# Kernel optimization log

Hardware: AMD Instinct MI355X
Metric: run time of the kernel (lower is better)

The kernel has to match this reference:

```python
import jax, jax.numpy as jnp
import numpy as np

NL, DM, DI, DS, DC, DR, NC = 4, 128, 256, 16, 4, 8, 10
ALPHA = 0.3  # observer_alpha

def layernorm(x, w, b, eps=1e-5):
    m = x.mean(-1, keepdims=True)
    v = ((x - m) ** 2).mean(-1, keepdims=True)
    return (x - m) / jnp.sqrt(v + eps) * w + b

def silu(x):
    return x * jax.nn.sigmoid(x)

def causal_dwconv(x, w, b):
    # x: (B, L, DI); w: (DI, 1, DC); b: (DI,)
    xt = x.transpose(0, 2, 1)  # (B, DI, L)
    y = jax.lax.conv_general_dilated(
        xt, w, window_strides=(1,), padding=[(DC - 1, 0)],
        dimension_numbers=('NCH', 'OIH', 'NCH'), feature_group_count=DI)
    return (y + b[None, :, None]).transpose(0, 2, 1)  # (B, L, DI)

def ssm_scan(delta, Bc, Cc, u, A):
    # delta, u: (B, L, DI); Bc, Cc: (B, L, DS); A: (DI, DS)
    B = delta.shape[0]
    def step(h, inp):
        d_t, b_t, c_t, u_t = inp  # (B,DI),(B,DS),(B,DS),(B,DI)
        dA = jnp.exp(d_t[..., None] * A)              # (B, DI, DS)
        h = dA * h + (d_t * u_t)[..., None] * b_t[:, None, :]
        y = jnp.einsum('bds,bs->bd', h, c_t)
        return h, y
    h0 = jnp.zeros((B, DI, DS), delta.dtype)
    xs = (delta.transpose(1, 0, 2), Bc.transpose(1, 0, 2),
          Cc.transpose(1, 0, 2), u.transpose(1, 0, 2))
    _, ys = jax.lax.scan(step, h0, xs)
    return ys.transpose(1, 0, 2)  # (B, L, DI)

def _forward(x, W_in, b_in, ln_w, ln_b, in_proj_w, conv_w, conv_b, x_proj_w,
             dt_proj_w, dt_proj_b, A_log, Dp, out_proj_w, out_proj_b,
             norm_w, norm_b, cls_w, cls_b):
    B = x.shape[0]
    u = x.transpose(0, 2, 3, 1).reshape(B, -1, 3)   # (B, L, 3)
    h = u @ W_in + b_in                              # (B, L, DM)
    for i in range(NL):
        res = h
        z = layernorm(h, ln_w[i], ln_b[i])
        xz = z @ in_proj_w[i]                        # (B, L, 2*DI)
        xin, gate = jnp.split(xz, 2, axis=-1)
        xc = silu(causal_dwconv(xin, conv_w[i], conv_b[i]))  # (B, L, DI)
        proj = xc @ x_proj_w[i]                      # (B, L, DR + 2*DS)
        dt, Bc, Cc = jnp.split(proj, [DR, DR + DS], axis=-1)
        delta = jax.nn.softplus(dt @ dt_proj_w[i] + dt_proj_b[i])  # (B, L, DI)
        A = -jnp.exp(A_log[i])                       # (DI, DS)
        y = ssm_scan(delta, Bc, Cc, xc, A) + xc * Dp[i]
        # Luenberger-style observer correction: blend predicted SSM output
        y = (1.0 - ALPHA) * y + ALPHA * xc
        y = y * silu(gate)
        h = res + y @ out_proj_w[i] + out_proj_b[i]
    pooled = h.mean(axis=1)                          # (B, DM)
    pooled = layernorm(pooled, norm_w, norm_b)
    return pooled @ cls_w + cls_b                    # (B, NC)

def setup_inputs():
    key = jax.random.key(0)
    ks = jax.random.split(key, 8)
    def nrm(k, shape, std=0.02):
        return jax.random.normal(k, shape, jnp.float32) * std
    return {
        'x': jax.random.normal(ks[0], (32, 3, 32, 32), jnp.float32),
        'W_in': nrm(ks[1], (3, DM)), 'b_in': jnp.zeros((DM,), jnp.float32),
        'ln_w': jnp.ones((NL, DM), jnp.float32), 'ln_b': jnp.zeros((NL, DM), jnp.float32),
        'in_proj_w': nrm(ks[2], (NL, DM, 2 * DI)),
        'conv_w': nrm(ks[3], (NL, DI, 1, DC), 0.2), 'conv_b': jnp.zeros((NL, DI), jnp.float32),
        'x_proj_w': nrm(ks[4], (NL, DI, DR + 2 * DS)),
        'dt_proj_w': nrm(ks[5], (NL, DR, DI), 0.1),
        'dt_proj_b': jnp.full((NL, DI), -4.6, jnp.float32),
        'A_log': jnp.log(jnp.broadcast_to(jnp.arange(1, DS + 1, dtype=jnp.float32), (NL, DI, DS))),
        'Dp': jnp.ones((NL, DI), jnp.float32),
        'out_proj_w': nrm(ks[6], (NL, DI, DM)), 'out_proj_b': jnp.zeros((NL, DM), jnp.float32),
        'norm_w': jnp.ones((DM,), jnp.float32), 'norm_b': jnp.zeros((DM,), jnp.float32),
        'cls_w': nrm(ks[7], (DM, NC)), 'cls_b': jnp.zeros((NC,), jnp.float32),
    }

def reference(x, W_in, b_in, ln_w, ln_b, in_proj_w, conv_w, conv_b, x_proj_w,
              dt_proj_w, dt_proj_b, A_log, Dp, out_proj_w, out_proj_b,
              norm_w, norm_b, cls_w, cls_b):
    return _forward(x, W_in, b_in, ln_w, ln_b, in_proj_w, conv_w, conv_b,
                    x_proj_w, dt_proj_w, dt_proj_b, A_log, Dp, out_proj_w,
                    out_proj_b, norm_w, norm_b, cls_w, cls_b)
```

## Files before the change

### kernel.cpp

```cpp
#include <hip/hip_runtime.h>
#include <math.h>

#define B_  32
#define L_  1024
#define T_  (B_ * L_)
#define DM_ 128
#define DI_ 256
#define DS_ 16
#define DC_ 4
#define DR_ 8
#define NC_ 10
#define CHUNK_ 32
#define NCH_  (L_ / CHUNK_)
#define PSTR_ 288

typedef __bf16 bf16x8 __attribute__((ext_vector_type(8)));
typedef __bf16 bf16x4 __attribute__((ext_vector_type(4)));
typedef __bf16 bf16x2 __attribute__((ext_vector_type(2)));
typedef float f32x4 __attribute__((ext_vector_type(4)));
typedef unsigned short u16x8 __attribute__((ext_vector_type(8)));

__device__ __forceinline__ float sigmoidf_(float x) { return 1.0f / (1.0f + __expf(-x)); }
__device__ __forceinline__ float siluf_(float x)    { return x * sigmoidf_(x); }
__device__ __forceinline__ float softplusf_(float x) {
    return (x > 15.0f) ? x : __logf(1.0f + __expf(x));
}
__device__ __forceinline__ float fexp2_(float x) { return __builtin_amdgcn_exp2f(x); }

__device__ __forceinline__ void gload_lds16(const __bf16* g, __bf16* l) {
    __builtin_amdgcn_global_load_lds(
        (const __attribute__((address_space(1))) void*)g,
        (__attribute__((address_space(3))) void*)l, 16, 0, 0);
}

template<int R>
__device__ __forceinline__ void stage_async(const __bf16* __restrict__ src,
        __bf16* lds, int k0, int stride, int wid, int lane) {
    constexpr int NI = R / 32;
#pragma unroll
    for (int j = 0; j < NI; ++j) {
        int s0 = (wid * NI + j) * 64;
        int s = s0 + lane;
        int row = s >> 3, sw = s & 7;
        int slot = sw ^ (row & 7);
        gload_lds16(src + (size_t)row * stride + k0 + slot * 8, lds + (size_t)s0 * 8);
    }
}

__global__ __launch_bounds__(128) void k_embed(const float* __restrict__ x,
        const float* __restrict__ Win, const float* __restrict__ bin,
        float* __restrict__ h) {
    int t = blockIdx.x;
    int b = t >> 10, l = t & 1023;
    int m = threadIdx.x;
    const float* xb = x + (size_t)b * 3 * 1024 + l;
    float acc = bin[m];
    acc = fmaf(xb[0],    Win[m],        acc);
    acc = fmaf(xb[1024], Win[128 + m],  acc);
    acc = fmaf(xb[2048], Win[256 + m],  acc);
    h[(size_t)t * 128 + m] = acc;
}

__global__ __launch_bounds__(256) void k_prep(const float* __restrict__ ipw,
        const float* __restrict__ opw, const float* __restrict__ xpw,
        const float* __restrict__ dtw, __bf16* __restrict__ wt1,
        __bf16* __restrict__ wt2, __bf16* __restrict__ wcat) {
    int blk = blockIdx.x;
    int tid = threadIdx.x;
    int i = blk * 256 + tid;
    if (i < 262144) {
        int lay = i >> 16, rem = i & 65535, n = rem >> 7, k = rem & 127;
        wt1[i] = (__bf16)ipw[lay * 65536 + k * 512 + n];
    }
    if (i < 131072) {
        int lay = i >> 15, rem = i & 32767, n = rem >> 8, k = rem & 255;
        wt2[i] = (__bf16)opw[lay * 32768 + k * 128 + n];
    }
    {
        int lay = blk / 384, n = blk % 384;
        int k = tid;
        float v;
        if (n < 256) {
            float acc = 0.0f;
#pragma unroll
            for (int r = 0; r < 8; ++r)
                acc = fmaf(xpw[lay * 10240 + k * 40 + r], dtw[lay * 2048 + r * 256 + n], acc);
            v = acc;
        } else if (n < 288) {
            v = xpw[lay * 10240 + k * 40 + (n - 248)];
        } else {
            v = 0.0f;
        }
        wcat[(size_t)blk * 256 + k] = (__bf16)v;
    }
}

__global__ __launch_bounds__(256) void k_ln(const float* __restrict__ h,
        const float* __restrict__ w, const float* __restrict__ b,
        __bf16* __restrict__ z) {
    int wid = threadIdx.x >> 6, lane = threadIdx.x & 63;
    int t = blockIdx.x * 4 + wid;
    const float* hr = h + (size_t)t * 128;
    float2 v = *(const float2*)(hr + lane * 2);
    float s = v.x + v.y, sq = v.x * v.x + v.y * v.y;
#pragma unroll
    for (int off = 1; off < 64; off <<= 1) {
        s += __shfl_xor(s, off);
        sq += __shfl_xor(sq, off);
    }
    float mean = s * (1.0f / 128.0f);
    float var = sq * (1.0f / 128.0f) - mean * mean;
    float rstd = rsqrtf(var + 1e-5f);
    float2 wv = *(const float2*)(w + lane * 2);
    float2 bv = *(const float2*)(b + lane * 2);
    bf16x2 o;
    o.x = (__bf16)((v.x - mean) * rstd * wv.x + bv.x);
    o.y = (__bf16)((v.y - mean) * rstd * wv.y + bv.y);
    *(bf16x2*)(z + (size_t)t * 128 + lane * 2) = o;
}

template<int BM, int K, int N, int MODE, bool GATE, bool WLN>
__global__ __launch_bounds__(256) void k_gemm_mfma(
        const __bf16* __restrict__ A, const __bf16* __restrict__ G,
        const __bf16* __restrict__ Wt, const float* __restrict__ bias,
        float* __restrict__ Cf, __bf16* __restrict__ Cb,
        const float* __restrict__ lnw, const float* __restrict__ lnb,
        __bf16* __restrict__ Zb) {
    static_assert(!GATE || BM == 32, "GATE staging assumes BM=32");
    static_assert(!WLN || (MODE == 2 && BM == 32 && N == 128), "WLN geometry");
    __shared__ __bf16 As[BM * 64];
    __shared__ __bf16 Bs[128 * 64];
    __shared__ float red_s[WLN ? 4 : 1][WLN ? 32 : 1];
    __shared__ float red_q[WLN ? 4 : 1][WLN ? 32 : 1];
    int tid = threadIdx.x;
    int bm = blockIdx.x, bn = blockIdx.y;
    int lane = tid & 63, wid = tid >> 6;
    int lr = lane & 15, lg = lane >> 4;
    constexpr int MF = BM / 16;

    f32x4 acc[MF][2] = {};
    const __bf16* Asrc = A + (size_t)(bm * BM) * K;
    const __bf16* Bsrc = Wt + (size_t)(bn * 128) * K;

    for (int k0 = 0; k0 < K; k0 += 64) {
        if (GATE) {
            int row = tid >> 3, slot = tid & 7;
            int m = bm * BM + row;
            bf16x8 yv = *(const bf16x8*)(A + (size_t)m * K + k0 + slot * 8);
            bf16x8 gv = *(const bf16x8*)(G + (size_t)m * 512 + 256 + k0 + slot * 8);
            bf16x8 v;
#pragma unroll
            for (int j = 0; j < 8; ++j)
                v[j] = (__bf16)((float)yv[j] * siluf_((float)gv[j]));
            *(bf16x8*)(As + row * 64 + ((slot ^ (row & 7)) * 8)) = v;
        } else {
            stage_async<BM>(Asrc, As, k0, K, wid, lane);
        }
        stage_async<128>(Bsrc, Bs, k0, K, wid, lane);
        __syncthreads();
#pragma unroll
        for (int ks = 0; ks < 2; ++ks) {
            int slotbase = ks * 4 + lg;
            bf16x8 af[MF], bfr[2];
#pragma unroll
            for (int m = 0; m < MF; ++m) {
                int row = m * 16 + lr;
                af[m] = *(const bf16x8*)(As + row * 64 + ((slotbase ^ (row & 7)) * 8));
            }
#pragma unroll
            for (int n = 0; n < 2; ++n) {
                int rn = wid * 32 + n * 16 + lr;
                bfr[n] = *(const bf16x8*)(Bs + rn * 64 + ((slotbase ^ (rn & 7)) * 8));
            }
#pragma unroll
            for (int m = 0; m < MF; ++m)
#pragma unroll
                for (int n = 0; n < 2; ++n)
                    acc[m][n] = __builtin_amdgcn_mfma_f32_16x16x32_bf16(
                        af[m], bfr[n], acc[m][n], 0, 0, 0);
        }
        __syncthreads();
    }
    float vv[MF][2][4];
#pragma unroll
    for (int m = 0; m < MF; ++m) {
#pragma unroll
        for (int n = 0; n < 2; ++n) {
            int col = bn * 128 + wid * 32 + n * 16 + lr;
            float bv = (MODE == 2) ? bias[col] : 0.0f;
            float dtbv = (MODE == 1 && col < 256) ? bias[col] : 0.0f;
#pragma unroll
            for (int rg = 0; rg < 4; ++rg) {
                int row = bm * BM + m * 16 + lg * 4 + rg;
                float v = acc[m][n][rg];
                if (MODE == 0) {
                    Cb[(size_t)row * N + col] = (__bf16)v;
                } else if (MODE == 1) {
                    if (col < 256)
                        Cb[(size_t)row * PSTR_ + col] = (__bf16)softplusf_(v + dtbv);
                    else if (col < 288)
                        Cb[(size_t)row * PSTR_ + col] = (__bf16)v;
                } else {
                    float* cp = Cf + (size_t)row * N + col;
                    v += *cp + bv;
                    *cp = v;
                    vv[m][n][rg] = v;
                }
            }
        }
    }
    if (WLN) {
        float ps[MF][4], pq[MF][4];
#pragma unroll
        for (int m = 0; m < MF; ++m)
#pragma unroll
            for (int rg = 0; rg < 4; ++rg) {
                float a = vv[m][0][rg], bv2 = vv[m][1][rg];
                ps[m][rg] = a + bv2;
                pq[m][rg] = a * a + bv2 * bv2;
            }
#pragma unroll
        for (int off = 1; off < 16; off <<= 1) {
#pragma unroll
            for (int m = 0; m < MF; ++m)
#pragma unroll
                for (int rg = 0; rg < 4; ++rg) {
                    ps[m][rg] += __shfl_xor(ps[m][rg], off);
                    pq[m][rg] += __shfl_xor(pq[m][rg], off);
                }
        }
        if (lr == 0) {
#pragma unroll
            for (int m = 0; m < MF; ++m)
#pragma unroll
                for (int rg = 0; rg < 4; ++rg) {
                    int rl = m * 16 + lg * 4 + rg;
                    red_s[wid][rl] = ps[m][rg];
                    red_q[wid][rl] = pq[m][rg];
                }
        }
        __syncthreads();
#pragma unroll
        for (int m = 0; m < MF; ++m)
#pragma unroll
            for (int rg = 0; rg < 4; ++rg) {
                int rl = m * 16 + lg * 4 + rg;
                float s = red_s[0][rl] + red_s[1][rl] + red_s[2][rl] + red_s[3][rl];
                float q = red_q[0][rl] + red_q[1][rl] + red_q[2][rl] + red_q[3][rl];
                float mean = s * (1.0f / 128.0f);
                float var = q * (1.0f / 128.0f) - mean * mean;
                float rstd = rsqrtf(var + 1e-5f);
#pragma unroll
                for (int n = 0; n < 2; ++n) {
                    int col = wid * 32 + n * 16 + lr;
                    float z = (vv[m][n][rg] - mean) * rstd * lnw[col] + lnb[col];
                    Zb[(size_t)(bm * BM + rl) * 128 + col] = (__bf16)z;
                }
            }
    }
}

__global__ __launch_bounds__(256) void k_conv(const __bf16* __restrict__ xzb,
        const float* __restrict__ cw, const float* __restrict__ cb,
        __bf16* __restrict__ xcb) {
    int t = blockIdx.x * 4 + (threadIdx.x >> 6);
    int d0 = (threadIdx.x & 63) * 4;
    int l = t & 1023;
    const __bf16* xp = xzb + (size_t)t * 512 + d0;
    float4 wv[4];
#pragma unroll
    for (int j = 0; j < 4; ++j) wv[j] = *(const float4*)(cw + (d0 + j) * 4);
    float acc[4] = {cb[d0], cb[d0 + 1], cb[d0 + 2], cb[d0 + 3]};
#pragma unroll
    for (int k = 0; k < 4; ++k) {
        int back = 3 - k;
        if (l >= back) {
            bf16x4 v = *(const bf16x4*)(xp - back * 512);
#pragma unroll
            for (int j = 0; j < 4; ++j)
                acc[j] = fmaf((float)v[j], ((const float*)&wv[j])[k], acc[j]);
        }
    }
    bf16x4 o;
#pragma unroll
    for (int j = 0; j < 4; ++j) o[j] = (__bf16)siluf_(acc[j]);
    *(bf16x4*)(xcb + (size_t)t * 256 + d0) = o;
}

template<bool FINAL>
__global__ __launch_bounds__(128) void k_scan_chunk(
        const __bf16* __restrict__ projall, const __bf16* __restrict__ xcb,
        const float* __restrict__ Alog, const float* __restrict__ Dp,
        float* __restrict__ P, float* __restrict__ S,
        __bf16* __restrict__ yb) {
    __shared__ unsigned du_lds[CHUNK_ * 128];
    __shared__ float bc[CHUNK_ * 32];
    int b = blockIdx.z, c = blockIdx.y, dg = blockIdx.x;
    int tid = threadIdx.x;
    int d = dg * 128 + tid;

    const __bf16* projC = projall + ((size_t)b * 1024 + c * CHUNK_) * PSTR_;
    const __bf16* xcC   = xcb + ((size_t)b * 1024 + c * CHUNK_) * 256 + dg * 128;

#pragma unroll
    for (int r = 0; r < (CHUNK_ * 16) / 128; ++r) {
        int item = r * 128 + tid;
        int t = item >> 4, o8 = (item & 15) * 8;
        u16x8 dv = *(const u16x8*)(projC + (size_t)t * PSTR_ + dg * 128 + o8);
        u16x8 xv = *(const u16x8*)(xcC + (size_t)t * 256 + o8);
        uint4 w0, w1;
        w0.x = dv[0] | ((unsigned)xv[0] << 16); w0.y = dv[1] | ((unsigned)xv[1] << 16);
        w0.z = dv[2] | ((unsigned)xv[2] << 16); w0.w = dv[3] | ((unsigned)xv[3] << 16);
        w1.x = dv[4] | ((unsigned)xv[4] << 16); w1.y = dv[5] | ((unsigned)xv[5] << 16);
        w1.z = dv[6] | ((unsigned)xv[6] << 16); w1.w = dv[7] | ((unsigned)xv[7] << 16);
        *(uint4*)(du_lds + t * 128 + o8)     = w0;
        *(uint4*)(du_lds + t * 128 + o8 + 4) = w1;
    }
#pragma unroll
    for (int r = 0; r < (CHUNK_ * 4) / 128; ++r) {
        int item = r * 128 + tid;
        int t = item >> 2, g8 = (item & 3) * 8;
        bf16x8 v = *(const bf16x8*)(projC + (size_t)t * PSTR_ + 256 + g8);
        float4 f0 = {(float)v[0], (float)v[1], (float)v[2], (float)v[3]};
        float4 f1 = {(float)v[4], (float)v[5], (float)v[6], (float)v[7]};
        *(float4*)(bc + t * 32 + g8)     = f0;
        *(float4*)(bc + t * 32 + g8 + 4) = f1;
    }

    float aa[16], hs[16];
#pragma unroll
    for (int jj = 0; jj < 4; ++jj) {
        float4 av = *(const float4*)(Alog + (size_t)d * 16 + jj * 4);
        aa[jj * 4 + 0] = -__expf(av.x) * 1.44269504088896f;
        aa[jj * 4 + 1] = -__expf(av.y) * 1.44269504088896f;
        aa[jj * 4 + 2] = -__expf(av.z) * 1.44269504088896f;
        aa[jj * 4 + 3] = -__expf(av.w) * 1.44269504088896f;
    }
    float Dpd = Dp[d];
    size_t psIdx = ((size_t)(b * NCH_ + c)) * 4096 + (size_t)d * 16;
    if (FINAL) {
#pragma unroll
        for (int jj = 0; jj < 4; ++jj) {
            float4 h0 = *(const float4*)(P + psIdx + jj * 4);
            hs[jj * 4 + 0] = h0.x; hs[jj * 4 + 1] = h0.y;
            hs[jj * 4 + 2] = h0.z; hs[jj * 4 + 3] = h0.w;
        }
    } else {
#pragma unroll
        for (int j = 0; j < 16; ++j) hs[j] = 0.0f;
    }
    float cumd = 0.0f;
    __bf16* yC = yb + ((size_t)b * 1024 + c * CHUNK_) * 256 + dg * 128 + tid;

    __syncthreads();
#pragma unroll 2
    for (int tt = 0; tt < CHUNK_; ++tt) {
        unsigned duv = du_lds[tt * 128 + tid];
        float delta_t = __uint_as_float(duv << 16);
        float u = __uint_as_float(duv & 0xffff0000u);
        float du = delta_t * u;
        const float* bcr = bc + tt * 32;
        if (!FINAL) cumd += delta_t;
        float ys = 0.0f;
#pragma unroll
        for (int jj = 0; jj < 4; ++jj) {
            float4 Bv = *(const float4*)(bcr + jj * 4);
            float4 Cv;
            if (FINAL) Cv = *(const float4*)(bcr + 16 + jj * 4);
#pragma unroll
            for (int j = 0; j < 4; ++j) {
                int s = jj * 4 + j;
                float dA = fexp2_(delta_t * aa[s]);
                hs[s] = fmaf(dA, hs[s], du * ((const float*)&Bv)[j]);
                if (FINAL) ys = fmaf(hs[s], ((const float*)&Cv)[j], ys);
            }
        }
        if (FINAL) {
            float yv = fmaf(u, Dpd, ys);
            yv = fmaf(0.7f, yv, 0.3f * u);
            yC[(size_t)tt * 256] = (__bf16)yv;
        }
    }
    if (!FINAL) {
#pragma unroll
        for (int jj = 0; jj < 4; ++jj) {
            float4 pv, sv;
            pv.x = fexp2_(aa[jj * 4 + 0] * cumd);
            pv.y = fexp2_(aa[jj * 4 + 1] * cumd);
            pv.z = fexp2_(aa[jj * 4 + 2] * cumd);
            pv.w = fexp2_(aa[jj * 4 + 3] * cumd);
            sv.x = hs[jj * 4 + 0]; sv.y = hs[jj * 4 + 1];
            sv.z = hs[jj * 4 + 2]; sv.w = hs[jj * 4 + 3];
            *(float4*)(P + psIdx + jj * 4) = pv;
            *(float4*)(S + psIdx + jj * 4) = sv;
        }
    }
}

__global__ __launch_bounds__(256) void k_scan_combine(float* __restrict__ P,
        const float* __restrict__ S) {
    int idx = blockIdx.x * 256 + threadIdx.x;
    int b = idx >> 12, rem = idx & 4095;
    float h = 0.0f;
#pragma unroll
    for (int c = 0; c < NCH_; ++c) {
        size_t base = ((size_t)(b * NCH_ + c)) * 4096 + rem;
        float p = P[base];
        float s = S[base];
        P[base] = h;
        h = fmaf(p, h, s);
    }
}

__global__ __launch_bounds__(128) void k_pool(const float* __restrict__ h,
        float* __restrict__ partial) {
    int b = blockIdx.x, lc = blockIdx.y;
    int m = threadIdx.x;
    const float* hb = h + (size_t)b * 131072 + (size_t)lc * 128 * 128 + m;
    float acc = 0.0f;
#pragma unroll 8
    for (int l = 0; l < 128; ++l) acc += hb[(size_t)l * 128];
    partial[((size_t)b * 8 + lc) * 128 + m] = acc;
}

__global__ __launch_bounds__(128) void k_head(const float* __restrict__ partial,
        const float* __restrict__ nw, const float* __restrict__ nb,
        const float* __restrict__ cw, const float* __restrict__ cb,
        float* __restrict__ out) {
    __shared__ float zs[128];
    __shared__ float red[128];
    int b = blockIdx.x, m = threadIdx.x;
    float v = 0.0f;
#pragma unroll
    for (int lc = 0; lc < 8; ++lc) v += partial[((size_t)b * 8 + lc) * 128 + m];
    v *= (1.0f / 1024.0f);
    red[m] = v;
    __syncthreads();
    for (int off = 64; off; off >>= 1) {
        if (m < off) red[m] += red[m + off];
        __syncthreads();
    }
    float mean = red[0] * (1.0f / 128.0f);
    __syncthreads();
    float dv = v - mean;
    red[m] = dv * dv;
    __syncthreads();
    for (int off = 64; off; off >>= 1) {
        if (m < off) red[m] += red[m + off];
        __syncthreads();
    }
    float rstd = rsqrtf(red[0] * (1.0f / 128.0f) + 1e-5f);
    zs[m] = dv * rstd * nw[m] + nb[m];
    __syncthreads();
    if (m < NC_) {
        float acc = cb[m];
#pragma unroll 8
        for (int k = 0; k < 128; ++k) acc = fmaf(zs[k], cw[k * 10 + m], acc);
        out[b * 10 + m] = acc;
    }
}

extern "C" void kernel_launch(void* const* d_in, const int* in_sizes, int n_in,
                              void* d_out, int out_size, void* d_ws, size_t ws_size,
                              hipStream_t stream) {
    const float* x    = (const float*)d_in[0];
    const float* Win  = (const float*)d_in[1];
    const float* bin  = (const float*)d_in[2];
    const float* lnw  = (const float*)d_in[3];
    const float* lnb  = (const float*)d_in[4];
    const float* ipw  = (const float*)d_in[5];
    const float* cw   = (const float*)d_in[6];
    const float* cb   = (const float*)d_in[7];
    const float* xpw  = (const float*)d_in[8];
    const float* dtw  = (const float*)d_in[9];
    const float* dtb  = (const float*)d_in[10];
    const float* Alog = (const float*)d_in[11];
    const float* Dp   = (const float*)d_in[12];
    const float* opw  = (const float*)d_in[13];
    const float* opb  = (const float*)d_in[14];
    const float* nw   = (const float*)d_in[15];
    const float* nb   = (const float*)d_in[16];
    const float* clw  = (const float*)d_in[17];
    const float* clb  = (const float*)d_in[18];

    float* ws = (float*)d_ws;
    float*  h       = ws;
    float*  P       = ws + 4194304;
    __bf16* zb      = (__bf16*)(ws + 4194304);
    __bf16* xzb     = (__bf16*)(ws + 8388608);
    __bf16* xcb     = (__bf16*)(ws + 16777216);
    __bf16* projall = (__bf16*)(ws + 20971520);
    __bf16* yb      = (__bf16*)(ws + 25690112);
    float*  partial = ws + 29884416;
    __bf16* wt1     = (__bf16*)(ws + 29917184);
    __bf16* wt2     = (__bf16*)(ws + 30048256);
    __bf16* wcat    = (__bf16*)(ws + 30113792);
    float*  Sb      = ws + 30310400;

    k_prep<<<1536, 256, 0, stream>>>(ipw, opw, xpw, dtw, wt1, wt2, wcat);
    k_embed<<<T_, 128, 0, stream>>>(x, Win, bin, h);
    k_ln<<<T_ / 4, 256, 0, stream>>>(h, lnw, lnb, zb);
    for (int lay = 0; lay < 4; ++lay) {
        k_gemm_mfma<64, 128, 512, 0, false, false><<<dim3(T_ / 64, 4), 256, 0, stream>>>(
            zb, nullptr, wt1 + (size_t)lay * 65536, nullptr, nullptr, xzb,
            nullptr, nullptr, nullptr);
        k_conv<<<T_ / 4, 256, 0, stream>>>(xzb, cw + lay * 1024, cb + lay * 256, xcb);
        k_gemm_mfma<64, 256, 384, 1, false, false><<<dim3(T_ / 64, 3), 256, 0, stream>>>(
            xcb, nullptr, wcat + (size_t)lay * 98304, dtb + lay * 256, nullptr, projall,
            nullptr, nullptr, nullptr);
        k_scan_chunk<false><<<dim3(2, NCH_, B_), 128, 0, stream>>>(projall, xcb,
            Alog + lay * 4096, Dp + lay * 256, P, Sb, yb);
        k_scan_combine<<<B_ * 4096 / 256, 256, 0, stream>>>(P, Sb);
        k_scan_chunk<true><<<dim3(2, NCH_, B_), 128, 0, stream>>>(projall, xcb,
            Alog + lay * 4096, Dp + lay * 256, P, Sb, yb);
        if (lay < 3) {
            k_gemm_mfma<32, 256, 128, 2, true, true><<<dim3(T_ / 32, 1), 256, 0, stream>>>(
                yb, xzb, wt2 + (size_t)lay * 32768, opb + lay * 128, h, nullptr,
                lnw + (lay + 1) * 128, lnb + (lay + 1) * 128, zb);
        } else {
            k_gemm_mfma<32, 256, 128, 2, true, false><<<dim3(T_ / 32, 1), 256, 0, stream>>>(
                yb, xzb, wt2 + (size_t)lay * 32768, opb + lay * 128, h, nullptr,
                nullptr, nullptr, nullptr);
        }
    }
    k_pool<<<dim3(32, 8), 128, 0, stream>>>(h, partial);
    k_head<<<32, 128, 0, stream>>>(partial, nw, nb, clw, clb, (float*)d_out);
}
```

Measured before the change: 617.2 us.

## Double-buffer LDS tiles in non-gated MFMA GEMM to overlap loads with compute

After: 617.4 us. Within noise of the previous version (+0.0%).

```diff
diff --git a/kernel.cpp b/kernel.cpp
--- a/kernel.cpp
+++ b/kernel.cpp
@@ -128,8 +128,9 @@
         __bf16* __restrict__ Zb) {
     static_assert(!GATE || BM == 32, "GATE staging assumes BM=32");
     static_assert(!WLN || (MODE == 2 && BM == 32 && N == 128), "WLN geometry");
-    __shared__ __bf16 As[BM * 64];
-    __shared__ __bf16 Bs[128 * 64];
+    constexpr int NBUF = GATE ? 1 : 2;
+    __shared__ __bf16 As[NBUF][BM * 64];
+    __shared__ __bf16 Bs[NBUF][128 * 64];
     __shared__ float red_s[WLN ? 4 : 1][WLN ? 32 : 1];
     __shared__ float red_q[WLN ? 4 : 1][WLN ? 32 : 1];
     int tid = threadIdx.x;
@@ -142,44 +143,83 @@
     const __bf16* Asrc = A + (size_t)(bm * BM) * K;
     const __bf16* Bsrc = Wt + (size_t)(bn * 128) * K;
 
-    for (int k0 = 0; k0 < K; k0 += 64) {
-        if (GATE) {
-            int row = tid >> 3, slot = tid & 7;
-            int m = bm * BM + row;
-            bf16x8 yv = *(const bf16x8*)(A + (size_t)m * K + k0 + slot * 8);
-            bf16x8 gv = *(const bf16x8*)(G + (size_t)m * 512 + 256 + k0 + slot * 8);
-            bf16x8 v;
-#pragma unroll
-            for (int j = 0; j < 8; ++j)
-                v[j] = (__bf16)((float)yv[j] * siluf_((float)gv[j]));
-            *(bf16x8*)(As + row * 64 + ((slot ^ (row & 7)) * 8)) = v;
-        } else {
-            stage_async<BM>(Asrc, As, k0, K, wid, lane);
-        }
-        stage_async<128>(Bsrc, Bs, k0, K, wid, lane);
-        __syncthreads();
-#pragma unroll
-        for (int ks = 0; ks < 2; ++ks) {
-            int slotbase = ks * 4 + lg;
-            bf16x8 af[MF], bfr[2];
-#pragma unroll
-            for (int m = 0; m < MF; ++m) {
-                int row = m * 16 + lr;
-                af[m] = *(const bf16x8*)(As + row * 64 + ((slotbase ^ (row & 7)) * 8));
-            }
-#pragma unroll
-            for (int n = 0; n < 2; ++n) {
-                int rn = wid * 32 + n * 16 + lr;
-                bfr[n] = *(const bf16x8*)(Bs + rn * 64 + ((slotbase ^ (rn & 7)) * 8));
-            }
-#pragma unroll
-            for (int m = 0; m < MF; ++m)
-#pragma unroll
-                for (int n = 0; n < 2; ++n)
-                    acc[m][n] = __builtin_amdgcn_mfma_f32_16x16x32_bf16(
-                        af[m], bfr[n], acc[m][n], 0, 0, 0);
-        }
-        __syncthreads();
+    if (!GATE) {
+        stage_async<BM>(Asrc, As[0], 0, K, wid, lane);
+        stage_async<128>(Bsrc, Bs[0], 0, K, wid, lane);
+        asm volatile("s_waitcnt vmcnt(0)" ::: "memory");
+        __builtin_amdgcn_s_barrier();
+        __builtin_amdgcn_sched_barrier(0);
+        int cur = 0;
+        for (int k0 = 0; k0 < K; k0 += 64) {
+            if (k0 + 64 < K) {
+                stage_async<BM>(Asrc, As[cur ^ 1], k0 + 64, K, wid, lane);
+                stage_async<128>(Bsrc, Bs[cur ^ 1], k0 + 64, K, wid, lane);
+            }
+            __builtin_amdgcn_sched_barrier(0);
+#pragma unroll
+            for (int ks = 0; ks < 2; ++ks) {
+                int slotbase = ks * 4 + lg;
+                bf16x8 af[MF], bfr[2];
+#pragma unroll
+                for (int m = 0; m < MF; ++m) {
+                    int row = m * 16 + lr;
+                    af[m] = *(const bf16x8*)(As[cur] + row * 64 + ((slotbase ^ (row & 7)) * 8));
+                }
+#pragma unroll
+                for (int n = 0; n < 2; ++n) {
+                    int rn = wid * 32 + n * 16 + lr;
+                    bfr[n] = *(const bf16x8*)(Bs[cur] + rn * 64 + ((slotbase ^ (rn & 7)) * 8));
+                }
+#pragma unroll
+                for (int m = 0; m < MF; ++m)
+#pragma unroll
+                    for (int n = 0; n < 2; ++n)
+                        acc[m][n] = __builtin_amdgcn_mfma_f32_16x16x32_bf16(
+                            af[m], bfr[n], acc[m][n], 0, 0, 0);
+            }
+            asm volatile("s_waitcnt vmcnt(0) lgkmcnt(0)" ::: "memory");
+            __builtin_amdgcn_s_barrier();
+            __builtin_amdgcn_sched_barrier(0);
+            cur ^= 1;
+        }
+    } else {
+        for (int k0 = 0; k0 < K; k0 += 64) {
+            {
+                int row = tid >> 3, slot = tid & 7;
+                int m = bm * BM + row;
+                bf16x8 yv = *(const bf16x8*)(A + (size_t)m * K + k0 + slot * 8);
+                bf16x8 gv = *(const bf16x8*)(G + (size_t)m * 512 + 256 + k0 + slot * 8);
+                bf16x8 v;
+#pragma unroll
+                for (int j = 0; j < 8; ++j)
+                    v[j] = (__bf16)((float)yv[j] * siluf_((float)gv[j]));
+                *(bf16x8*)(As[0] + row * 64 + ((slot ^ (row & 7)) * 8)) = v;
+            }
+            stage_async<128>(Bsrc, Bs[0], k0, K, wid, lane);
+            __syncthreads();
+#pragma unroll
+            for (int ks = 0; ks < 2; ++ks) {
+                int slotbase = ks * 4 + lg;
+                bf16x8 af[MF], bfr[2];
+#pragma unroll
+                for (int m = 0; m < MF; ++m) {
+                    int row = m * 16 + lr;
+                    af[m] = *(const bf16x8*)(As[0] + row * 64 + ((slotbase ^ (row & 7)) * 8));
+                }
+#pragma unroll
+                for (int n = 0; n < 2; ++n) {
+                    int rn = wid * 32 + n * 16 + lr;
+                    bfr[n] = *(const bf16x8*)(Bs[0] + rn * 64 + ((slotbase ^ (rn & 7)) * 8));
+                }
+#pragma unroll
+                for (int m = 0; m < MF; ++m)
+#pragma unroll
+                    for (int n = 0; n < 2; ++n)
+                        acc[m][n] = __builtin_amdgcn_mfma_f32_16x16x32_bf16(
+                            af[m], bfr[n], acc[m][n], 0, 0, 0);
+            }
+            __syncthreads();
+        }
     }
     float vv[MF][2][4];
 #pragma unroll
```

## Compute delta projection inside scan; shrink x_proj GEMM and pre-silu gate

Applied to the files above, without the earlier changes.

Result: no change. 621.2 us (+0.6%).

```diff
diff --git a/kernel.cpp b/kernel.cpp
--- a/kernel.cpp
+++ b/kernel.cpp
@@ -12,13 +12,12 @@
 #define NC_ 10
 #define CHUNK_ 32
 #define NCH_  (L_ / CHUNK_)
-#define PSTR_ 288
+#define PSTR_ 64
 
 typedef __bf16 bf16x8 __attribute__((ext_vector_type(8)));
 typedef __bf16 bf16x4 __attribute__((ext_vector_type(4)));
 typedef __bf16 bf16x2 __attribute__((ext_vector_type(2)));
 typedef float f32x4 __attribute__((ext_vector_type(4)));
-typedef unsigned short u16x8 __attribute__((ext_vector_type(8)));
 
 __device__ __forceinline__ float sigmoidf_(float x) { return 1.0f / (1.0f + __expf(-x)); }
 __device__ __forceinline__ float siluf_(float x)    { return x * sigmoidf_(x); }
@@ -63,12 +62,12 @@
 
 __global__ __launch_bounds__(256) void k_prep(const float* __restrict__ ipw,
         const float* __restrict__ opw, const float* __restrict__ xpw,
-        const float* __restrict__ dtw, __bf16* __restrict__ wt1,
-        __bf16* __restrict__ wt2, __bf16* __restrict__ wcat) {
+        __bf16* __restrict__ wt1, __bf16* __restrict__ wt2,
+        __bf16* __restrict__ wcat) {
     int blk = blockIdx.x;
     int tid = threadIdx.x;
     int i = blk * 256 + tid;
-    if (i < 262144) {
+    {
         int lay = i >> 16, rem = i & 65535, n = rem >> 7, k = rem & 127;
         wt1[i] = (__bf16)ipw[lay * 65536 + k * 512 + n];
     }
@@ -76,21 +75,10 @@
         int lay = i >> 15, rem = i & 32767, n = rem >> 8, k = rem & 255;
         wt2[i] = (__bf16)opw[lay * 32768 + k * 128 + n];
     }
-    {
-        int lay = blk / 384, n = blk % 384;
+    if (blk < 256) {
+        int lay = blk >> 6, n = blk & 63;
         int k = tid;
-        float v;
-        if (n < 256) {
-            float acc = 0.0f;
-#pragma unroll
-            for (int r = 0; r < 8; ++r)
-                acc = fmaf(xpw[lay * 10240 + k * 40 + r], dtw[lay * 2048 + r * 256 + n], acc);
-            v = acc;
-        } else if (n < 288) {
-            v = xpw[lay * 10240 + k * 40 + (n - 248)];
-        } else {
-            v = 0.0f;
-        }
+        float v = (n < 40) ? xpw[lay * 10240 + k * 40 + n] : 0.0f;
         wcat[(size_t)blk * 256 + k] = (__bf16)v;
     }
 }
@@ -147,11 +135,11 @@
             int row = tid >> 3, slot = tid & 7;
             int m = bm * BM + row;
             bf16x8 yv = *(const bf16x8*)(A + (size_t)m * K + k0 + slot * 8);
-            bf16x8 gv = *(const bf16x8*)(G + (size_t)m * 512 + 256 + k0 + slot * 8);
+            bf16x8 gv = *(const bf16x8*)(G + (size_t)m * 256 + k0 + slot * 8);
             bf16x8 v;
 #pragma unroll
             for (int j = 0; j < 8; ++j)
-                v[j] = (__bf16)((float)yv[j] * siluf_((float)gv[j]));
+                v[j] = (__bf16)((float)yv[j] * (float)gv[j]);
             *(bf16x8*)(As + row * 64 + ((slot ^ (row & 7)) * 8)) = v;
         } else {
             stage_async<BM>(Asrc, As, k0, K, wid, lane);
@@ -188,17 +176,17 @@
         for (int n = 0; n < 2; ++n) {
             int col = bn * 128 + wid * 32 + n * 16 + lr;
             float bv = (MODE == 2) ? bias[col] : 0.0f;
-            float dtbv = (MODE == 1 && col < 256) ? bias[col] : 0.0f;
 #pragma unroll
             for (int rg = 0; rg < 4; ++rg) {
                 int row = bm * BM + m * 16 + lg * 4 + rg;
                 float v = acc[m][n][rg];
                 if (MODE == 0) {
-                    Cb[(size_t)row * N + col] = (__bf16)v;
+                    if (col < 256)
+                        Cb[(size_t)row * 256 + col] = (__bf16)v;
+                    else
+                        Zb[(size_t)row * 256 + (col - 256)] = (__bf16)siluf_(v);
                 } else if (MODE == 1) {
-                    if (col < 256)
-                        Cb[(size_t)row * PSTR_ + col] = (__bf16)softplusf_(v + dtbv);
-                    else if (col < 288)
+                    if (col < 40)
                         Cb[(size_t)row * PSTR_ + col] = (__bf16)v;
                 } else {
                     float* cp = Cf + (size_t)row * N + col;
@@ -260,13 +248,13 @@
     }
 }
 
-__global__ __launch_bounds__(256) void k_conv(const __bf16* __restrict__ xzb,
+__global__ __launch_bounds__(256) void k_conv(const __bf16* __restrict__ xinb,
         const float* __restrict__ cw, const float* __restrict__ cb,
         __bf16* __restrict__ xcb) {
     int t = blockIdx.x * 4 + (threadIdx.x >> 6);
     int d0 = (threadIdx.x & 63) * 4;
     int l = t & 1023;
-    const __bf16* xp = xzb + (size_t)t * 512 + d0;
+    const __bf16* xp = xinb + (size_t)t * 256 + d0;
     float4 wv[4];
 #pragma unroll
     for (int j = 0; j < 4; ++j) wv[j] = *(const float4*)(cw + (d0 + j) * 4);
@@ -275,7 +263,7 @@
     for (int k = 0; k < 4; ++k) {
         int back = 3 - k;
         if (l >= back) {
-            bf16x4 v = *(const bf16x4*)(xp - back * 512);
+            bf16x4 v = *(const bf16x4*)(xp - back * 256);
 #pragma unroll
             for (int j = 0; j < 4; ++j)
                 acc[j] = fmaf((float)v[j], ((const float*)&wv[j])[k], acc[j]);
@@ -290,11 +278,13 @@
 template<bool FINAL>
 __global__ __launch_bounds__(128) void k_scan_chunk(
         const __bf16* __restrict__ projall, const __bf16* __restrict__ xcb,
+        const float* __restrict__ dtw, const float* __restrict__ dtb,
         const float* __restrict__ Alog, const float* __restrict__ Dp,
         float* __restrict__ P, float* __restrict__ S,
         __bf16* __restrict__ yb) {
-    __shared__ unsigned du_lds[CHUNK_ * 128];
+    __shared__ __bf16 xcs[CHUNK_ * 128];
     __shared__ float bc[CHUNK_ * 32];
+    __shared__ float dts[CHUNK_ * 8];
     int b = blockIdx.z, c = blockIdx.y, dg = blockIdx.x;
     int tid = threadIdx.x;
     int d = dg * 128 + tid;
@@ -306,27 +296,26 @@
     for (int r = 0; r < (CHUNK_ * 16) / 128; ++r) {
         int item = r * 128 + tid;
         int t = item >> 4, o8 = (item & 15) * 8;
-        u16x8 dv = *(const u16x8*)(projC + (size_t)t * PSTR_ + dg * 128 + o8);
-        u16x8 xv = *(const u16x8*)(xcC + (size_t)t * 256 + o8);
-        uint4 w0, w1;
-        w0.x = dv[0] | ((unsigned)xv[0] << 16); w0.y = dv[1] | ((unsigned)xv[1] << 16);
-        w0.z = dv[2] | ((unsigned)xv[2] << 16); w0.w = dv[3] | ((unsigned)xv[3] << 16);
-        w1.x = dv[4] | ((unsigned)xv[4] << 16); w1.y = dv[5] | ((unsigned)xv[5] << 16);
-        w1.z = dv[6] | ((unsigned)xv[6] << 16); w1.w = dv[7] | ((unsigned)xv[7] << 16);
-        *(uint4*)(du_lds + t * 128 + o8)     = w0;
-        *(uint4*)(du_lds + t * 128 + o8 + 4) = w1;
-    }
-#pragma unroll
-    for (int r = 0; r < (CHUNK_ * 4) / 128; ++r) {
-        int item = r * 128 + tid;
-        int t = item >> 2, g8 = (item & 3) * 8;
-        bf16x8 v = *(const bf16x8*)(projC + (size_t)t * PSTR_ + 256 + g8);
+        *(bf16x8*)(xcs + t * 128 + o8) = *(const bf16x8*)(xcC + (size_t)t * 256 + o8);
+    }
+    {
+        int t = tid >> 2, g8 = (tid & 3) * 8;
+        bf16x8 v = *(const bf16x8*)(projC + (size_t)t * PSTR_ + 8 + g8);
         float4 f0 = {(float)v[0], (float)v[1], (float)v[2], (float)v[3]};
         float4 f1 = {(float)v[4], (float)v[5], (float)v[6], (float)v[7]};
         *(float4*)(bc + t * 32 + g8)     = f0;
         *(float4*)(bc + t * 32 + g8 + 4) = f1;
     }
-
+    if (tid < CHUNK_) {
+        bf16x8 v = *(const bf16x8*)(projC + (size_t)tid * PSTR_);
+#pragma unroll
+        for (int j = 0; j < 8; ++j) dts[tid * 8 + j] = (float)v[j];
+    }
+
+    float dtwc[8];
+#pragma unroll
+    for (int r = 0; r < 8; ++r) dtwc[r] = dtw[r * 256 + d];
+    float dtbd = dtb[d];
     float aa[16], hs[16];
 #pragma unroll
     for (int jj = 0; jj < 4; ++jj) {
@@ -355,9 +344,16 @@
     __syncthreads();
 #pragma unroll 2
     for (int tt = 0; tt < CHUNK_; ++tt) {
-        unsigned duv = du_lds[tt * 128 + tid];
-        float delta_t = __uint_as_float(duv << 16);
-        float u = __uint_as_float(duv & 0xffff0000u);
+        const float* dtr = dts + tt * 8;
+        float4 dt0 = *(const float4*)(dtr);
+        float4 dt1 = *(const float4*)(dtr + 4);
+        float dtv = dtbd;
+        dtv = fmaf(dt0.x, dtwc[0], dtv); dtv = fmaf(dt0.y, dtwc[1], dtv);
+        dtv = fmaf(dt0.z, dtwc[2], dtv); dtv = fmaf(dt0.w, dtwc[3], dtv);
+        dtv = fmaf(dt1.x, dtwc[4], dtv); dtv = fmaf(dt1.y, dtwc[5], dtv);
+        dtv = fmaf(dt1.z, dtwc[6], dtv); dtv = fmaf(dt1.w, dtwc[7], dtv);
+        float delta_t = softplusf_(dtv);
+        float u = (float)xcs[tt * 128 + tid];
         float du = delta_t * u;
         const float* bcr = bc + tt * 32;
         if (!FINAL) cumd += delta_t;
@@ -487,7 +483,8 @@
     float*  h       = ws;
     float*  P       = ws + 4194304;
     __bf16* zb      = (__bf16*)(ws + 4194304);
-    __bf16* xzb     = (__bf16*)(ws + 8388608);
+    __bf16* xinb    = (__bf16*)(ws + 8388608);
+    __bf16* sgb     = (__bf16*)(ws + 12582912);
     __bf16* xcb     = (__bf16*)(ws + 16777216);
     __bf16* projall = (__bf16*)(ws + 20971520);
     __bf16* yb      = (__bf16*)(ws + 25690112);
@@ -497,29 +494,31 @@
     __bf16* wcat    = (__bf16*)(ws + 30113792);
     float*  Sb      = ws + 30310400;
 
-    k_prep<<<1536, 256, 0, stream>>>(ipw, opw, xpw, dtw, wt1, wt2, wcat);
+    k_prep<<<1024, 256, 0, stream>>>(ipw, opw, xpw, wt1, wt2, wcat);
     k_embed<<<T_, 128, 0, stream>>>(x, Win, bin, h);
     k_ln<<<T_ / 4, 256, 0, stream>>>(h, lnw, lnb, zb);
     for (int lay = 0; lay < 4; ++lay) {
         k_gemm_mfma<64, 128, 512, 0, false, false><<<dim3(T_ / 64, 4), 256, 0, stream>>>(
-            zb, nullptr, wt1 + (size_t)lay * 65536, nullptr, nullptr, xzb,
-            nullptr, nullptr, nullptr);
-        k_conv<<<T_ / 4, 256, 0, stream>>>(xzb, cw + lay * 1024, cb + lay * 256, xcb);
-        k_gemm_mfma<64, 256, 384, 1, false, false><<<dim3(T_ / 64, 3), 256, 0, stream>>>(
-            xcb, nullptr, wcat + (size_t)lay * 98304, dtb + lay * 256, nullptr, projall,
+            zb, nullptr, wt1 + (size_t)lay * 65536, nullptr, nullptr, xinb,
+            nullptr, nullptr, sgb);
+        k_conv<<<T_ / 4, 256, 0, stream>>>(xinb, cw + lay * 1024, cb + lay * 256, xcb);
+        k_gemm_mfma<64, 256, 128, 1, false, false><<<dim3(T_ / 64, 1), 256, 0, stream>>>(
+            xcb, nullptr, wcat + (size_t)lay * 16384, nullptr, nullptr, projall,
             nullptr, nullptr, nullptr);
         k_scan_chunk<false><<<dim3(2, NCH_, B_), 128, 0, stream>>>(projall, xcb,
-            Alog + lay * 4096, Dp + lay * 256, P, Sb, yb);
+            dtw + lay * 2048, dtb + lay * 256, Alog + lay * 4096, Dp + lay * 256,
+            P, Sb, yb);
         k_scan_combine<<<B_ * 4096 / 256, 256, 0, stream>>>(P, Sb);
         k_scan_chunk<true><<<dim3(2, NCH_, B_), 128, 0, stream>>>(projall, xcb,
-            Alog + lay * 4096, Dp + lay * 256, P, Sb, yb);
+            dtw + lay * 2048, dtb + lay * 256, Alog + lay * 4096, Dp + lay * 256,
+            P, Sb, yb);
         if (lay < 3) {
             k_gemm_mfma<32, 256, 128, 2, true, true><<<dim3(T_ / 32, 1), 256, 0, stream>>>(
-                yb, xzb, wt2 + (size_t)lay * 32768, opb + lay * 128, h, nullptr,
+                yb, sgb, wt2 + (size_t)lay * 32768, opb + lay * 128, h, nullptr,
                 lnw + (lay + 1) * 128, lnb + (lay + 1) * 128, zb);
         } else {
             k_gemm_mfma<32, 256, 128, 2, true, false><<<dim3(T_ / 32, 1), 256, 0, stream>>>(
-                yb, xzb, wt2 + (size_t)lay * 32768, opb + lay * 128, h, nullptr,
+                yb, sgb, wt2 + (size_t)lay * 32768, opb + lay * 128, h, nullptr,
                 nullptr, nullptr, nullptr);
         }
     }
```
